# Performance work log

Measured on AMD Instinct MI355X. Metric: run time of the kernel, lower is better.

The kernel has to match this reference:

```python
import jax, jax.numpy as jnp
import numpy as np

BINS = 10
LOSS_WEIGHT = 1.0
N, C = 524288, 80


def setup_inputs() -> dict:
    key = jax.random.key(0)
    k1, k2 = jax.random.split(key)
    pred = jax.random.normal(k1, (N, C), dtype=jnp.float32)
    target = jax.random.randint(k2, (N, C), 0, 2).astype(jnp.float32)
    label_weight = jnp.ones((N, C), dtype=jnp.float32)
    return {"pred": pred, "target": target, "label_weight": label_weight}


def reference(pred, target, label_weight):
    # gradient magnitude g = |sigmoid(pred).detach() - target|, in [0, 1)
    g = jnp.abs(jax.nn.sigmoid(jax.lax.stop_gradient(pred)) - target)
    valid = (label_weight > 0)
    validf = valid.astype(pred.dtype)
    tot = jnp.maximum(jnp.sum(validf), 1.0)

    # edges[i] = i/BINS (last edge nudged by 1e-6) -> bin index = floor(g*BINS), clipped
    idx = jnp.clip(jnp.floor(g * BINS).astype(jnp.int32), 0, BINS - 1)
    counts = jnp.zeros((BINS,), dtype=pred.dtype).at[idx.ravel()].add(validf.ravel())
    nonempty = counts > 0
    n = jnp.sum(nonempty.astype(pred.dtype))

    w_per_bin = jnp.where(nonempty, tot / jnp.maximum(counts, 1.0), 0.0)
    weights = w_per_bin[idx] * validf
    weights = weights / jnp.maximum(n, 1.0)
    weights = jax.lax.stop_gradient(weights)  # weights carry no grad in the original

    # binary_cross_entropy_with_logits, elementwise, stable form
    bce = jnp.maximum(pred, 0.0) - pred * target + jnp.log1p(jnp.exp(-jnp.abs(pred)))
    loss = jnp.sum(weights * bce) / tot
    return loss * LOSS_WEIGHT
```

## Files before the change

### kernel.cpp

```cpp
#include <hip/hip_runtime.h>
#include <math.h>

#define BINS 10
#define REPL 16

struct WS {
    double       sum[BINS];
    unsigned int cnt[BINS];
};

__device__ __forceinline__ void accum_one(float x, float t, float w, int r,
                                          float* s_sum, unsigned int* s_cnt) {
    if (!(w > 0.0f)) return;
    float ax  = fabsf(x);
    float e   = __expf(-ax);
    float inv = __builtin_amdgcn_rcpf(1.0f + e);
    float sig = (x >= 0.0f) ? inv : (1.0f - inv);
    float g   = fabsf(sig - t);
    int idx   = (int)(g * 10.0f);
    idx = idx > (BINS - 1) ? (BINS - 1) : (idx < 0 ? 0 : idx);
    float bce = fmaxf(x, 0.0f) - x * t + __logf(1.0f + e);
    atomicAdd(&s_sum[idx * REPL + r], bce);
    atomicAdd(&s_cnt[idx * REPL + r], 1u);
}

__global__ __launch_bounds__(256) void ghmc_main(const float* __restrict__ pred,
                                                 const float* __restrict__ target,
                                                 const float* __restrict__ lw,
                                                 WS* __restrict__ ws,
                                                 long long total) {
    __shared__ float        s_sum[BINS * REPL];
    __shared__ unsigned int s_cnt[BINS * REPL];
    const int tid = threadIdx.x;
    for (int i = tid; i < BINS * REPL; i += blockDim.x) { s_sum[i] = 0.0f; s_cnt[i] = 0u; }
    __syncthreads();

    const int r = tid & (REPL - 1);
    const long long nvec   = total >> 2;
    const long long stride = (long long)gridDim.x * blockDim.x;

    for (long long i = (long long)blockIdx.x * blockDim.x + tid; i < nvec; i += stride) {
        float4 p = reinterpret_cast<const float4*>(pred)[i];
        float4 t = reinterpret_cast<const float4*>(target)[i];
        float4 w = reinterpret_cast<const float4*>(lw)[i];
        float px[4] = {p.x, p.y, p.z, p.w};
        float tx[4] = {t.x, t.y, t.z, t.w};
        float wx[4] = {w.x, w.y, w.z, w.w};
#pragma unroll
        for (int k = 0; k < 4; ++k)
            accum_one(px[k], tx[k], wx[k], r, s_sum, s_cnt);
    }

    const long long base = nvec << 2;
    const int rem = (int)(total - base);
    if (blockIdx.x == 0 && tid < rem)
        accum_one(pred[base + tid], target[base + tid], lw[base + tid], r, s_sum, s_cnt);

    __syncthreads();
    if (tid < BINS) {
        float s = 0.0f; unsigned int c = 0u;
#pragma unroll
        for (int j = 0; j < REPL; ++j) { s += s_sum[tid * REPL + j]; c += s_cnt[tid * REPL + j]; }
        if (c) {
            atomicAdd(&ws->sum[tid], (double)s);
            atomicAdd(&ws->cnt[tid], c);
        }
    }
}

__global__ void ghmc_finalize(const WS* __restrict__ ws, float* __restrict__ out) {
    if (threadIdx.x == 0 && blockIdx.x == 0) {
        double acc = 0.0;
        int n = 0;
        for (int b = 0; b < BINS; ++b) {
            unsigned int c = ws->cnt[b];
            if (c) { acc += ws->sum[b] / (double)c; ++n; }
        }
        double denom = (n > 0) ? (double)n : 1.0;
        out[0] = (float)(acc / denom);
    }
}

extern "C" void kernel_launch(void* const* d_in, const int* in_sizes, int n_in,
                              void* d_out, int out_size, void* d_ws, size_t ws_size,
                              hipStream_t stream) {
    const float* pred   = (const float*)d_in[0];
    const float* target = (const float*)d_in[1];
    const float* lw     = (const float*)d_in[2];
    float* out = (float*)d_out;
    WS* ws = (WS*)d_ws;
    const long long total = (long long)in_sizes[0];

    hipMemsetAsync(d_ws, 0, sizeof(WS), stream);

    const int threads = 256;
    const int blocks  = 2048;
    ghmc_main<<<blocks, threads, 0, stream>>>(pred, target, lw, ws, total);
    ghmc_finalize<<<1, 64, 0, stream>>>(ws, out);
}
```

Baseline: 514.8 us.

## Replace shared-memory atomic histogram with per-thread register bins and wave reductions

Each thread now keeps the 10 bin sums and counts in registers, updating them with predicated selects instead of LDS atomics. The bins are then combined with wavefront shuffles and a small shared-memory step, and each block writes its own partial record, so the global double atomics and the memset are gone. A parallel finalize kernel reduces the 2048 partials. This removes LDS atomic contention in the memory-bound loop, at the cost of more VALU work per element and more register pressure.

```diff
diff --git a/kernel.cpp b/kernel.cpp
--- a/kernel.cpp
+++ b/kernel.cpp
@@ -2,82 +2,138 @@
 #include <math.h>
 
 #define BINS 10
-#define REPL 16
+#define NBLOCKS 2048
+#define THREADS 256
 
-struct WS {
-    double       sum[BINS];
+struct Partial {
+    float        sum[BINS];
     unsigned int cnt[BINS];
 };
 
-__device__ __forceinline__ void accum_one(float x, float t, float w, int r,
-                                          float* s_sum, unsigned int* s_cnt) {
-    if (!(w > 0.0f)) return;
+__device__ __forceinline__ void accum_one(float x, float t, float w,
+                                          float (&s)[BINS], unsigned int (&c)[BINS]) {
+    const bool valid = (w > 0.0f);
     float ax  = fabsf(x);
     float e   = __expf(-ax);
     float inv = __builtin_amdgcn_rcpf(1.0f + e);
     float sig = (x >= 0.0f) ? inv : (1.0f - inv);
     float g   = fabsf(sig - t);
     int idx   = (int)(g * 10.0f);
-    idx = idx > (BINS - 1) ? (BINS - 1) : (idx < 0 ? 0 : idx);
+    idx = idx > (BINS - 1) ? (BINS - 1) : idx;
     float bce = fmaxf(x, 0.0f) - x * t + __logf(1.0f + e);
-    atomicAdd(&s_sum[idx * REPL + r], bce);
-    atomicAdd(&s_cnt[idx * REPL + r], 1u);
+    bce = valid ? bce : 0.0f;
+    const unsigned int one = valid ? 1u : 0u;
+#pragma unroll
+    for (int b = 0; b < BINS; ++b) {
+        const bool m = (idx == b);
+        s[b] += m ? bce : 0.0f;
+        c[b] += m ? one : 0u;
+    }
 }
 
-__global__ __launch_bounds__(256) void ghmc_main(const float* __restrict__ pred,
-                                                 const float* __restrict__ target,
-                                                 const float* __restrict__ lw,
-                                                 WS* __restrict__ ws,
-                                                 long long total) {
-    __shared__ float        s_sum[BINS * REPL];
-    __shared__ unsigned int s_cnt[BINS * REPL];
+__global__ __launch_bounds__(THREADS) void ghmc_main(const float* __restrict__ pred,
+                                                     const float* __restrict__ target,
+                                                     const float* __restrict__ lw,
+                                                     Partial* __restrict__ part,
+                                                     long long total) {
+    float        s[BINS];
+    unsigned int c[BINS];
+#pragma unroll
+    for (int b = 0; b < BINS; ++b) { s[b] = 0.0f; c[b] = 0u; }
+
     const int tid = threadIdx.x;
-    for (int i = tid; i < BINS * REPL; i += blockDim.x) { s_sum[i] = 0.0f; s_cnt[i] = 0u; }
-    __syncthreads();
+    const long long nvec   = total >> 2;
+    const long long stride = (long long)gridDim.x * THREADS;
 
-    const int r = tid & (REPL - 1);
-    const long long nvec   = total >> 2;
-    const long long stride = (long long)gridDim.x * blockDim.x;
-
-    for (long long i = (long long)blockIdx.x * blockDim.x + tid; i < nvec; i += stride) {
+    for (long long i = (long long)blockIdx.x * THREADS + tid; i < nvec; i += stride) {
         float4 p = reinterpret_cast<const float4*>(pred)[i];
         float4 t = reinterpret_cast<const float4*>(target)[i];
         float4 w = reinterpret_cast<const float4*>(lw)[i];
-        float px[4] = {p.x, p.y, p.z, p.w};
-        float tx[4] = {t.x, t.y, t.z, t.w};
-        float wx[4] = {w.x, w.y, w.z, w.w};
-#pragma unroll
-        for (int k = 0; k < 4; ++k)
-            accum_one(px[k], tx[k], wx[k], r, s_sum, s_cnt);
+        accum_one(p.x, t.x, w.x, s, c);
+        accum_one(p.y, t.y, w.y, s, c);
+        accum_one(p.z, t.z, w.z, s, c);
+        accum_one(p.w, t.w, w.w, s, c);
     }
 
     const long long base = nvec << 2;
     const int rem = (int)(total - base);
     if (blockIdx.x == 0 && tid < rem)
-        accum_one(pred[base + tid], target[base + tid], lw[base + tid], r, s_sum, s_cnt);
+        accum_one(pred[base + tid], target[base + tid], lw[base + tid], s, c);
 
+#pragma unroll
+    for (int b = 0; b < BINS; ++b) {
+#pragma unroll
+        for (int off = 32; off; off >>= 1) {
+            s[b] += __shfl_xor(s[b], off, 64);
+            c[b] += __shfl_xor(c[b], off, 64);
+        }
+    }
+
+    __shared__ float        ls[THREADS / 64][BINS];
+    __shared__ unsigned int lc[THREADS / 64][BINS];
+    const int wid  = tid >> 6;
+    const int lane = tid & 63;
+    if (lane == 0) {
+#pragma unroll
+        for (int b = 0; b < BINS; ++b) { ls[wid][b] = s[b]; lc[wid][b] = c[b]; }
+    }
     __syncthreads();
+
     if (tid < BINS) {
-        float s = 0.0f; unsigned int c = 0u;
+        float sb = 0.0f; unsigned int cb = 0u;
 #pragma unroll
-        for (int j = 0; j < REPL; ++j) { s += s_sum[tid * REPL + j]; c += s_cnt[tid * REPL + j]; }
-        if (c) {
-            atomicAdd(&ws->sum[tid], (double)s);
-            atomicAdd(&ws->cnt[tid], c);
-        }
+        for (int w2 = 0; w2 < THREADS / 64; ++w2) { sb += ls[w2][tid]; cb += lc[w2][tid]; }
+        part[blockIdx.x].sum[tid] = sb;
+        part[blockIdx.x].cnt[tid] = cb;
     }
 }
 
-__global__ void ghmc_finalize(const WS* __restrict__ ws, float* __restrict__ out) {
-    if (threadIdx.x == 0 && blockIdx.x == 0) {
-        double acc = 0.0;
+__global__ __launch_bounds__(THREADS) void ghmc_finalize(const Partial* __restrict__ part,
+                                                         float* __restrict__ out,
+                                                         int nblocks) {
+    double             acc[BINS];
+    unsigned long long cn[BINS];
+#pragma unroll
+    for (int b = 0; b < BINS; ++b) { acc[b] = 0.0; cn[b] = 0ull; }
+
+    const int tid = threadIdx.x;
+    for (int i = tid; i < nblocks; i += THREADS) {
+#pragma unroll
+        for (int b = 0; b < BINS; ++b) {
+            acc[b] += (double)part[i].sum[b];
+            cn[b]  += (unsigned long long)part[i].cnt[b];
+        }
+    }
+
+#pragma unroll
+    for (int b = 0; b < BINS; ++b) {
+#pragma unroll
+        for (int off = 32; off; off >>= 1) {
+            acc[b] += __shfl_xor(acc[b], off, 64);
+            cn[b]  += __shfl_xor(cn[b], off, 64);
+        }
+    }
+
+    __shared__ double             lds_s[THREADS / 64][BINS];
+    __shared__ unsigned long long lds_c[THREADS / 64][BINS];
+    const int wid  = tid >> 6;
+    const int lane = tid & 63;
+    if (lane == 0) {
+#pragma unroll
+        for (int b = 0; b < BINS; ++b) { lds_s[wid][b] = acc[b]; lds_c[wid][b] = cn[b]; }
+    }
+    __syncthreads();
+
+    if (tid == 0) {
+        double loss = 0.0;
         int n = 0;
         for (int b = 0; b < BINS; ++b) {
-            unsigned int c = ws->cnt[b];
-            if (c) { acc += ws->sum[b] / (double)c; ++n; }
+            double sb = 0.0; unsigned long long cb = 0ull;
+            for (int w2 = 0; w2 < THREADS / 64; ++w2) { sb += lds_s[w2][b]; cb += lds_c[w2][b]; }
+            if (cb) { loss += sb / (double)cb; ++n; }
         }
         double denom = (n > 0) ? (double)n : 1.0;
-        out[0] = (float)(acc / denom);
+        out[0] = (float)(loss / denom);
     }
 }
 
@@ -88,13 +144,9 @@
     const float* target = (const float*)d_in[1];
     const float* lw     = (const float*)d_in[2];
     float* out = (float*)d_out;
-    WS* ws = (WS*)d_ws;
+    Partial* part = (Partial*)d_ws;
     const long long total = (long long)in_sizes[0];
 
-    hipMemsetAsync(d_ws, 0, sizeof(WS), stream);
-
-    const int threads = 256;
-    const int blocks  = 2048;
-    ghmc_main<<<blocks, threads, 0, stream>>>(pred, target, lw, ws, total);
-    ghmc_finalize<<<1, 64, 0, stream>>>(ws, out);
+    ghmc_main<<<NBLOCKS, THREADS, 0, stream>>>(pred, target, lw, part, total);
+    ghmc_finalize<<<1, THREADS, 0, stream>>>(part, out, NBLOCKS);
 }
```

After: 458.3 us. 11.0% less time.
